# Performance work log

Measured on AMD Instinct MI355X. Metric: run time of the kernel, lower is better.

The kernel has to match this reference:

```python
import jax, jax.numpy as jnp
import numpy as np

B, TQ, TKV, D, H = 4, 512, 4096, 1024, 8
HEAD_DIM = D // H


def setup_inputs() -> dict:
    key = jax.random.key(0)
    ks = jax.random.split(key, 8)
    s = 0.02
    inputs_q = jax.random.normal(ks[0], (B, TQ, D), jnp.float32)
    inputs_kv = jax.random.normal(ks[1], (B, TKV, D), jnp.float32)
    attention_mask = jax.random.randint(ks[2], (B, TQ, TKV), 0, 2).astype(bool)
    Wq = jax.random.normal(ks[3], (D, D), jnp.float32) * s
    Wk = jax.random.normal(ks[4], (D, D), jnp.float32) * s
    Wv = jax.random.normal(ks[5], (D, D), jnp.float32) * s
    Wo = jax.random.normal(ks[6], (D, D), jnp.float32) * s
    zb = jnp.zeros((D,), jnp.float32)
    return {"inputs_q": inputs_q, "inputs_kv": inputs_kv, "attention_mask": attention_mask,
            "Wq": Wq, "bq": zb, "Wk": Wk, "bk": zb, "Wv": Wv, "bv": zb, "Wo": Wo, "bo": zb}


def _split_heads(x, h):
    b, t, c = x.shape
    return x.reshape(b, t, h, c // h).transpose(0, 2, 1, 3)  # b h t d


def reference(inputs_q, inputs_kv, attention_mask, Wq, bq, Wk, bk, Wv, bv, Wo, bo):
    q = _split_heads(inputs_q @ Wq + bq, H)   # [b,h,tq,d]
    k = _split_heads(inputs_kv @ Wk + bk, H)  # [b,h,tkv,d]
    v = _split_heads(inputs_kv @ Wv + bv, H)  # [b,h,tkv,d]
    scale = 1.0 / np.sqrt(HEAD_DIM).astype(np.float32)
    scores = jnp.einsum('bhtd,bhTd->bhtT', q, k) * scale
    large_k = jnp.asarray(1e30, scores.dtype)  # 1e30 for fp32 per source
    scores = jnp.where(attention_mask[:, None, :, :], scores, -large_k)
    probs = jax.nn.softmax(scores, axis=-1)
    summed = jnp.einsum('bhtT,bhTd->bhtd', probs, v)
    b, h, t, d = summed.shape
    summed = summed.transpose(0, 2, 1, 3).reshape(b, t, h * d)  # [b,tq,hiddens]
    # wipe rows whose mask is entirely zero (post-softmax wipe-masking)
    wipe = jnp.all(~attention_mask, axis=-1, keepdims=True)  # [b,tq,1]
    summed = jnp.where(wipe, jnp.zeros_like(summed), summed)
    return summed @ Wo + bo
```

## Files before the change

kernel.cpp:

```cpp
#include <hip/hip_runtime.h>
#include <cstdint>
#include <cstddef>

typedef unsigned short US;
typedef __bf16 bf16_t;
typedef bf16_t bf16x8 __attribute__((ext_vector_type(8)));
typedef float  f32x4  __attribute__((ext_vector_type(4)));
typedef US     us8    __attribute__((ext_vector_type(8)));
typedef US     us4    __attribute__((ext_vector_type(4)));

#define AS1 __attribute__((address_space(1)))
#define AS3 __attribute__((address_space(3)))

__device__ __forceinline__ void gl_lds16(const void* g, void* l) {
    __builtin_amdgcn_global_load_lds((AS1 unsigned int*)(size_t)g,
                                     (AS3 unsigned int*)l, 16, 0, 0);
}

__device__ __forceinline__ US f2bf(float f) {
    unsigned u = __builtin_bit_cast(unsigned, f);
    u += 0x7FFFu + ((u >> 16) & 1u);
    return (US)(u >> 16);
}

__device__ __forceinline__ bf16x8 ldv8(const US* p) {
    return __builtin_bit_cast(bf16x8, *(const us8*)p);
}

__global__ void conv_bf16(const float* __restrict__ in, US* __restrict__ out, int n4) {
    int i = blockIdx.x * blockDim.x + threadIdx.x;
    if (i < n4) {
        float4 f = ((const float4*)in)[i];
        us4 o = { f2bf(f.x), f2bf(f.y), f2bf(f.z), f2bf(f.w) };
        ((us4*)out)[i] = o;
    }
}

__global__ void conv_mask(const int* __restrict__ in, US* __restrict__ out, int n4) {
    int i = blockIdx.x * blockDim.x + threadIdx.x;
    if (i < n4) {
        int4 m = ((const int4*)in)[i];
        us4 o = { (US)(m.x ? 1 : 0), (US)(m.y ? 1 : 0),
                  (US)(m.z ? 1 : 0), (US)(m.w ? 1 : 0) };
        ((us4*)out)[i] = o;
    }
}

__global__ void wt_conv(const float* __restrict__ Wq, const float* __restrict__ Wk,
                        const float* __restrict__ Wv, const float* __restrict__ Wo,
                        US* __restrict__ outbase) {
    const float* W = (blockIdx.z == 0) ? Wq : (blockIdx.z == 1) ? Wk
                   : (blockIdx.z == 2) ? Wv : Wo;
    US* WT = outbase + (size_t)blockIdx.z * 1024 * 1024;
    __shared__ float t[32][33];
    int tx = threadIdx.x & 31, ty = threadIdx.x >> 5;
    int x = blockIdx.x * 32 + tx;
#pragma unroll
    for (int r = 0; r < 4; ++r)
        t[ty + r * 8][tx] = W[(size_t)(blockIdx.y * 32 + ty + r * 8) * 1024 + x];
    __syncthreads();
    int nx = blockIdx.y * 32 + tx;
#pragma unroll
    for (int r = 0; r < 4; ++r)
        WT[(size_t)(blockIdx.x * 32 + ty + r * 8) * 1024 + nx] = f2bf(t[tx][ty + r * 8]);
}

__global__ void v_transpose(const US* __restrict__ Vh, US* __restrict__ VTh) {
    __shared__ US t[32][33];
    int tx = threadIdx.x & 31, ty = threadIdx.x >> 5;
    size_t base = (size_t)blockIdx.z * 4096 * 128;
    int t0 = blockIdx.x * 32, d0 = blockIdx.y * 32;
#pragma unroll
    for (int r = 0; r < 4; ++r)
        t[ty + r * 8][tx] = Vh[base + (size_t)(t0 + ty + r * 8) * 128 + d0 + tx];
    __syncthreads();
#pragma unroll
    for (int r = 0; r < 4; ++r)
        VTh[base + (size_t)(d0 + ty + r * 8) * 4096 + t0 + tx] = t[tx][ty + r * 8];
}

template <int MODE>
__global__ __launch_bounds__(256, 2)
void gemm_bt(const US* __restrict__ A, const US* __restrict__ Bt,
             const float* __restrict__ bias, void* __restrict__ out,
             int tlog2, float scale) {
    constexpr int K = 1024, N = 1024, BK = 64;
    __shared__ US As[128 * BK];
    __shared__ US Bs[128 * BK];
    const int tid = threadIdx.x;
    const int wv = tid >> 6, ln = tid & 63;
    const int g = ln >> 4, c15 = ln & 15;
    const int m0 = blockIdx.x * 128, n0 = blockIdx.y * 128;
    const int wm = (wv & 1) * 64, wn = (wv >> 1) * 64;

    f32x4 acc[4][4];
    const f32x4 z = {0.f, 0.f, 0.f, 0.f};
#pragma unroll
    for (int i = 0; i < 4; ++i)
#pragma unroll
        for (int j = 0; j < 4; ++j) acc[i][j] = z;

    const US* Ab = A + (size_t)m0 * K;
    const US* Bb = Bt + (size_t)n0 * K;

    for (int k0 = 0; k0 < K; k0 += BK) {
        __syncthreads();
#pragma unroll
        for (int q = 0; q < 4; ++q) {
            int eb = (q * 256 + wv * 64) * 8;
            int r = (eb >> 6) + (ln >> 3);
            int sw = (ln & 7) ^ (r & 7);
            gl_lds16(Ab + (size_t)r * K + k0 + sw * 8, &As[eb]);
            gl_lds16(Bb + (size_t)r * K + k0 + sw * 8, &Bs[eb]);
        }
        __syncthreads();
#pragma unroll
        for (int ks = 0; ks < 2; ++ks) {
            bf16x8 a[4], b[4];
#pragma unroll
            for (int i = 0; i < 4; ++i) {
                int p = (ks * 4 + g) ^ (c15 & 7);
                a[i] = ldv8(&As[(wm + i * 16 + c15) * BK + p * 8]);
            }
#pragma unroll
            for (int j = 0; j < 4; ++j) {
                int p = (ks * 4 + g) ^ (c15 & 7);
                b[j] = ldv8(&Bs[(wn + j * 16 + c15) * BK + p * 8]);
            }
#pragma unroll
            for (int i = 0; i < 4; ++i)
#pragma unroll
                for (int j = 0; j < 4; ++j)
                    acc[i][j] = __builtin_amdgcn_mfma_f32_16x16x32_bf16(a[i], b[j], acc[i][j], 0, 0, 0);
        }
    }

#pragma unroll
    for (int i = 0; i < 4; ++i) {
#pragma unroll
        for (int j = 0; j < 4; ++j) {
            int col = n0 + wn + j * 16 + c15;
            float bvv = bias[col];
#pragma unroll
            for (int r = 0; r < 4; ++r) {
                int row = m0 + wm + i * 16 + g * 4 + r;
                float v = (acc[i][j][r] + bvv) * scale;
                if (MODE == 0) {
                    int b_ = row >> tlog2;
                    int t = row & ((1 << tlog2) - 1);
                    int h = col >> 7, d = col & 127;
                    ((US*)out)[(((size_t)(b_ * 8 + h) << tlog2) + t) * 128 + d] = f2bf(v);
                } else {
                    ((float*)out)[(size_t)row * N + col] = v;
                }
            }
        }
    }
}

__global__ __launch_bounds__(256, 2)
void gemm_kv(const US* __restrict__ A, const US* __restrict__ BtK,
             const US* __restrict__ BtV, const float* __restrict__ bk,
             const float* __restrict__ bv, US* __restrict__ Kout,
             US* __restrict__ Vout) {
    constexpr int K = 1024, BK = 64;
    __shared__ US As[128 * BK];
    __shared__ US BsK[128 * BK];
    __shared__ US BsV[128 * BK];
    const int tid = threadIdx.x;
    const int wv = tid >> 6, ln = tid & 63;
    const int g = ln >> 4, c15 = ln & 15;
    const int m0 = blockIdx.x * 128, n0 = blockIdx.y * 128;
    const int wm = (wv & 1) * 64, wn = (wv >> 1) * 64;

    f32x4 aK[4][4], aV[4][4];
    const f32x4 z = {0.f, 0.f, 0.f, 0.f};
#pragma unroll
    for (int i = 0; i < 4; ++i)
#pragma unroll
        for (int j = 0; j < 4; ++j) { aK[i][j] = z; aV[i][j] = z; }

    const US* Ab  = A   + (size_t)m0 * K;
    const US* BbK = BtK + (size_t)n0 * K;
    const US* BbV = BtV + (size_t)n0 * K;

    for (int k0 = 0; k0 < K; k0 += BK) {
        __syncthreads();
#pragma unroll
        for (int q = 0; q < 4; ++q) {
            int eb = (q * 256 + wv * 64) * 8;
            int r = (eb >> 6) + (ln >> 3);
            int sw = (ln & 7) ^ (r & 7);
            gl_lds16(Ab  + (size_t)r * K + k0 + sw * 8, &As[eb]);
            gl_lds16(BbK + (size_t)r * K + k0 + sw * 8, &BsK[eb]);
            gl_lds16(BbV + (size_t)r * K + k0 + sw * 8, &BsV[eb]);
        }
        __syncthreads();
#pragma unroll
        for (int ks = 0; ks < 2; ++ks) {
            bf16x8 a[4], bK[4], bV[4];
#pragma unroll
            for (int i = 0; i < 4; ++i) {
                int p = (ks * 4 + g) ^ (c15 & 7);
                a[i] = ldv8(&As[(wm + i * 16 + c15) * BK + p * 8]);
            }
#pragma unroll
            for (int j = 0; j < 4; ++j) {
                int p = (ks * 4 + g) ^ (c15 & 7);
                bK[j] = ldv8(&BsK[(wn + j * 16 + c15) * BK + p * 8]);
                bV[j] = ldv8(&BsV[(wn + j * 16 + c15) * BK + p * 8]);
            }
#pragma unroll
            for (int i = 0; i < 4; ++i)
#pragma unroll
                for (int j = 0; j < 4; ++j) {
                    aK[i][j] = __builtin_amdgcn_mfma_f32_16x16x32_bf16(a[i], bK[j], aK[i][j], 0, 0, 0);
                    aV[i][j] = __builtin_amdgcn_mfma_f32_16x16x32_bf16(a[i], bV[j], aV[i][j], 0, 0, 0);
                }
        }
    }

#pragma unroll
    for (int i = 0; i < 4; ++i) {
#pragma unroll
        for (int j = 0; j < 4; ++j) {
            int col = n0 + wn + j * 16 + c15;
            float bkv = bk[col], bvv = bv[col];
            int h = col >> 7, d = col & 127;
#pragma unroll
            for (int r = 0; r < 4; ++r) {
                int row = m0 + wm + i * 16 + g * 4 + r;
                int b_ = row >> 12, t = row & 4095;
                size_t oi = (((size_t)(b_ * 8 + h) << 12) + t) * 128 + d;
                Kout[oi] = f2bf(aK[i][j][r] + bkv);
                Vout[oi] = f2bf(aV[i][j][r] + bvv);
            }
        }
    }
}

__global__ __launch_bounds__(256, 3)
void flash(const US* __restrict__ Qh, const US* __restrict__ Kh,
           const US* __restrict__ VTh, const US* __restrict__ Mk,
           float* __restrict__ Opart, float* __restrict__ Lpart) {
    __shared__ US Ks[64 * 128];
    __shared__ US Vs[128 * 64];
    __shared__ US Qs[64 * 128];
    const int tid = threadIdx.x, wv = tid >> 6, ln = tid & 63;
    const int g = ln >> 4, c15 = ln & 15;
    const int qt = blockIdx.x, q0 = qt * 64;
    const int bh = blockIdx.y, b_ = bh >> 3;
    const int sp = blockIdx.z, kvbase = sp * 1024;
    const int wq = wv * 16;

    {
        const US* Qb = Qh + ((size_t)bh * 512 + q0) * 128;
#pragma unroll
        for (int q = 0; q < 4; ++q) {
            int eb = (q * 256 + wv * 64) * 8;
            int r = (eb >> 7) + (ln >> 4);
            int sw = (ln & 15) ^ (r & 15);
            gl_lds16(Qb + (size_t)r * 128 + sw * 8, &Qs[eb]);
        }
    }
    __syncthreads();
    bf16x8 qa[4];
#pragma unroll
    for (int s = 0; s < 4; ++s) {
        int p = (s * 4 + g) ^ c15;
        qa[s] = ldv8(&Qs[(wq + c15) * 128 + p * 8]);
    }
    __syncthreads();
    US* Pw = &Qs[wv * (16 * 64)];

    f32x4 o[8];
    const f32x4 z = {0.f, 0.f, 0.f, 0.f};
#pragma unroll
    for (int j = 0; j < 8; ++j) o[j] = z;
    float l4[4] = {0.f, 0.f, 0.f, 0.f};

    const US* mrow  = Mk + (size_t)(b_ * 512 + q0 + wq + g * 4) * 4096 + c15;
    const US* Kbase = Kh + (size_t)bh * 4096 * 128;
    const US* Vbase = VTh + (size_t)bh * 128 * 4096;

    for (int t = 0; t < 16; ++t) {
        int kv0 = kvbase + t * 64;
        __syncthreads();
        const US* Kb = Kbase + (size_t)kv0 * 128;
#pragma unroll
        for (int q = 0; q < 4; ++q) {
            int eb = (q * 256 + wv * 64) * 8;
            int r = (eb >> 7) + (ln >> 4);
            int sw = (ln & 15) ^ (r & 15);
            gl_lds16(Kb + (size_t)r * 128 + sw * 8, &Ks[eb]);
        }
#pragma unroll
        for (int q = 0; q < 4; ++q) {
            int eb = (q * 256 + wv * 64) * 8;
            int r = (eb >> 6) + (ln >> 3);
            int sw = (ln & 7) ^ (r & 7);
            gl_lds16(Vbase + (size_t)r * 4096 + kv0 + sw * 8, &Vs[eb]);
        }
        US mv[4][4];
#pragma unroll
        for (int r2 = 0; r2 < 4; ++r2) {
            const US* pr = mrow + (size_t)r2 * 4096 + kv0;
#pragma unroll
            for (int j = 0; j < 4; ++j) mv[r2][j] = pr[j * 16];
        }
        __syncthreads();

        f32x4 s[4];
#pragma unroll
        for (int j = 0; j < 4; ++j) s[j] = z;
#pragma unroll
        for (int ks = 0; ks < 4; ++ks) {
#pragma unroll
            for (int j = 0; j < 4; ++j) {
                int p = (ks * 4 + g) ^ c15;
                bf16x8 kb = ldv8(&Ks[(j * 16 + c15) * 128 + p * 8]);
                s[j] = __builtin_amdgcn_mfma_f32_16x16x32_bf16(qa[ks], kb, s[j], 0, 0, 0);
            }
        }
#pragma unroll
        for (int j = 0; j < 4; ++j) {
#pragma unroll
            for (int r2 = 0; r2 < 4; ++r2) {
                float pp = __expf(s[j][r2]);
                pp = mv[r2][j] ? pp : 0.0f;
                l4[r2] += pp;
                int m = g * 4 + r2;
                int c = (c15 >> 3) + j * 2;
                Pw[m * 64 + ((c ^ (m & 7)) * 8) + (c15 & 7)] = f2bf(pp);
            }
        }
#pragma unroll
        for (int ks = 0; ks < 2; ++ks) {
            int pp_ = (ks * 4 + g) ^ (c15 & 7);
            bf16x8 pa = ldv8(&Pw[c15 * 64 + pp_ * 8]);
#pragma unroll
            for (int j = 0; j < 8; ++j) {
                int pv = (ks * 4 + g) ^ (c15 & 7);
                bf16x8 vb = ldv8(&Vs[(j * 16 + c15) * 64 + pv * 8]);
                o[j] = __builtin_amdgcn_mfma_f32_16x16x32_bf16(pa, vb, o[j], 0, 0, 0);
            }
        }
    }

#pragma unroll
    for (int r = 0; r < 4; ++r) {
        float l = l4[r];
        l += __shfl_xor(l, 1); l += __shfl_xor(l, 2);
        l += __shfl_xor(l, 4); l += __shfl_xor(l, 8);
        l4[r] = l;
    }
    size_t obase = ((((size_t)sp * 32 + bh) * 8 + qt) * 64 + wq) * 128;
#pragma unroll
    for (int j = 0; j < 8; ++j)
#pragma unroll
        for (int r = 0; r < 4; ++r)
            Opart[obase + (size_t)(g * 4 + r) * 128 + j * 16 + c15] = o[j][r];
    if (c15 == 0) {
#pragma unroll
        for (int r = 0; r < 4; ++r)
            Lpart[(((size_t)sp * 32 + bh) * 8 + qt) * 64 + wq + g * 4 + r] = l4[r];
    }
}

__global__ void combine(const float* __restrict__ Opart, const float* __restrict__ Lpart,
                        US* __restrict__ AO) {
    const int bh = blockIdx.x >> 3, qt = blockIdx.x & 7;
    const int b_ = bh >> 3, h = bh & 7;
    const int tid = threadIdx.x;
    const size_t sstride = (size_t)32 * 8 * 64 * 128;
    const size_t lstride = (size_t)32 * 8 * 64;
    const size_t slice  = ((size_t)bh * 8 + qt) * 64 * 128;
    const size_t lslice = ((size_t)bh * 8 + qt) * 64;
#pragma unroll
    for (int i = 0; i < 8; ++i) {
        int p = tid + i * 256;
        int row = p >> 5;
        float lsum = Lpart[lslice + row] + Lpart[lstride + lslice + row]
                   + Lpart[2 * lstride + lslice + row] + Lpart[3 * lstride + lslice + row];
        float inv = lsum > 0.f ? 1.f / lsum : 0.f;
        float4 a = *((const float4*)(Opart + slice) + p);
        float4 b = *((const float4*)(Opart + sstride + slice) + p);
        float4 c = *((const float4*)(Opart + 2 * sstride + slice) + p);
        float4 d = *((const float4*)(Opart + 3 * sstride + slice) + p);
        float x = (a.x + b.x + c.x + d.x) * inv;
        float y = (a.y + b.y + c.y + d.y) * inv;
        float z2 = (a.z + b.z + c.z + d.z) * inv;
        float w = (a.w + b.w + c.w + d.w) * inv;
        int d_ = (p & 31) * 4;
        int trow = qt * 64 + row;
        us4 ov = { f2bf(x), f2bf(y), f2bf(z2), f2bf(w) };
        *(us4*)(AO + ((size_t)(b_ * 512 + trow)) * 1024 + h * 128 + d_) = ov;
    }
}

extern "C" void kernel_launch(void* const* d_in, const int* in_sizes, int n_in,
                              void* d_out, int out_size, void* d_ws, size_t ws_size,
                              hipStream_t stream) {
    (void)in_sizes; (void)n_in; (void)out_size; (void)ws_size;
    const float* Xq  = (const float*)d_in[0];
    const float* Xkv = (const float*)d_in[1];
    const int*   Mi  = (const int*)d_in[2];
    const float* Wq  = (const float*)d_in[3];
    const float* bq  = (const float*)d_in[4];
    const float* Wk  = (const float*)d_in[5];
    const float* bk  = (const float*)d_in[6];
    const float* Wv  = (const float*)d_in[7];
    const float* bv  = (const float*)d_in[8];
    const float* Wo  = (const float*)d_in[9];
    const float* bo  = (const float*)d_in[10];
    float* out = (float*)d_out;

    char* p = (char*)d_ws;
    US* XqB  = (US*)p; p += (size_t)2048 * 1024 * 2;
    US* XkvB = (US*)p; p += (size_t)16384 * 1024 * 2;
    US* WT   = (US*)p; p += (size_t)4 * 1024 * 1024 * 2;
    US* MB   = (US*)p; p += (size_t)4 * 512 * 4096 * 2;
    US* Qh   = (US*)p; p += (size_t)2048 * 1024 * 2;
    US* Kh   = (US*)p; p += (size_t)16384 * 1024 * 2;
    US* Vh   = (US*)p; p += (size_t)16384 * 1024 * 2;
    US* VTh  = (US*)p; p += (size_t)16384 * 1024 * 2;
    US* AO   = (US*)p; p += (size_t)2048 * 1024 * 2;
    float* Opart = (float*)XkvB;
    float* Lpart = (float*)Vh;

    conv_bf16<<<2048, 256, 0, stream>>>(Xq, XqB, 2048 * 1024 / 4);
    conv_bf16<<<16384, 256, 0, stream>>>(Xkv, XkvB, 16384 * 1024 / 4);
    conv_mask<<<8192, 256, 0, stream>>>(Mi, MB, 4 * 512 * 4096 / 4);
    wt_conv<<<dim3(32, 32, 4), 256, 0, stream>>>(Wq, Wk, Wv, Wo, WT);

    gemm_bt<0><<<dim3(16, 8), 256, 0, stream>>>(XqB, WT, bq, Qh, 9, 0.08838834764831843f);
    gemm_kv<<<dim3(128, 8), 256, 0, stream>>>(XkvB, WT + 1048576, WT + 2097152,
                                              bk, bv, Kh, Vh);
    v_transpose<<<dim3(128, 4, 32), 256, 0, stream>>>(Vh, VTh);
    flash<<<dim3(8, 32, 4), 256, 0, stream>>>(Qh, Kh, VTh, MB, Opart, Lpart);
    combine<<<256, 256, 0, stream>>>(Opart, Lpart, AO);
    gemm_bt<1><<<dim3(16, 8), 256, 0, stream>>>(AO, WT + 3145728, bo, out, 0, 1.0f);
}
```

Before: 382.3 us.

## Widen flash q-tile to 128, split KV six ways, fuse prep kernels

The flash kernel now gives each wave 32 query rows instead of 16, so every K/V tile loaded into LDS is reused across twice as many queries. Q fragments are loaded straight from global memory, and the KV range is split into 6 uneven chunks to keep the grid size reasonable. Partial outputs are stored transposed with vectorized mask loads, and combine uses an LDS transpose to reduce 6 partials. The three conversion kernels are merged into one launch. The cost is higher register pressure, since the kernel holds twice the accumulators, plus extra combine traffic from 6 partials instead of 4.

```diff
diff --git a/kernel.cpp b/kernel.cpp
--- a/kernel.cpp
+++ b/kernel.cpp
@@ -27,22 +27,26 @@
     return __builtin_bit_cast(bf16x8, *(const us8*)p);
 }
 
-__global__ void conv_bf16(const float* __restrict__ in, US* __restrict__ out, int n4) {
-    int i = blockIdx.x * blockDim.x + threadIdx.x;
-    if (i < n4) {
-        float4 f = ((const float4*)in)[i];
+__global__ void prep(const float* __restrict__ Xq, const float* __restrict__ Xkv,
+                     const int* __restrict__ Mi, US* __restrict__ XqB,
+                     US* __restrict__ XkvB, US* __restrict__ MB) {
+    int b = blockIdx.x, tid = threadIdx.x;
+    if (b < 2048) {
+        int i = b * 256 + tid;
+        float4 f = ((const float4*)Xq)[i];
         us4 o = { f2bf(f.x), f2bf(f.y), f2bf(f.z), f2bf(f.w) };
-        ((us4*)out)[i] = o;
-    }
-}
-
-__global__ void conv_mask(const int* __restrict__ in, US* __restrict__ out, int n4) {
-    int i = blockIdx.x * blockDim.x + threadIdx.x;
-    if (i < n4) {
-        int4 m = ((const int4*)in)[i];
+        ((us4*)XqB)[i] = o;
+    } else if (b < 18432) {
+        int i = (b - 2048) * 256 + tid;
+        float4 f = ((const float4*)Xkv)[i];
+        us4 o = { f2bf(f.x), f2bf(f.y), f2bf(f.z), f2bf(f.w) };
+        ((us4*)XkvB)[i] = o;
+    } else {
+        int i = (b - 18432) * 256 + tid;
+        int4 m = ((const int4*)Mi)[i];
         us4 o = { (US)(m.x ? 1 : 0), (US)(m.y ? 1 : 0),
                   (US)(m.z ? 1 : 0), (US)(m.w ? 1 : 0) };
-        ((us4*)out)[i] = o;
+        ((us4*)MB)[i] = o;
     }
 }
 
@@ -245,48 +249,42 @@
            float* __restrict__ Opart, float* __restrict__ Lpart) {
     __shared__ US Ks[64 * 128];
     __shared__ US Vs[128 * 64];
-    __shared__ US Qs[64 * 128];
+    __shared__ US Ps[4][32 * 64];
     const int tid = threadIdx.x, wv = tid >> 6, ln = tid & 63;
     const int g = ln >> 4, c15 = ln & 15;
-    const int qt = blockIdx.x, q0 = qt * 64;
+    const int qt = blockIdx.x, qbase = qt * 128;
     const int bh = blockIdx.y, b_ = bh >> 3;
-    const int sp = blockIdx.z, kvbase = sp * 1024;
-    const int wq = wv * 16;
-
-    {
-        const US* Qb = Qh + ((size_t)bh * 512 + q0) * 128;
-#pragma unroll
-        for (int q = 0; q < 4; ++q) {
-            int eb = (q * 256 + wv * 64) * 8;
-            int r = (eb >> 7) + (ln >> 4);
-            int sw = (ln & 15) ^ (r & 15);
-            gl_lds16(Qb + (size_t)r * 128 + sw * 8, &Qs[eb]);
-        }
-    }
-    __syncthreads();
-    bf16x8 qa[4];
-#pragma unroll
-    for (int s = 0; s < 4; ++s) {
-        int p = (s * 4 + g) ^ c15;
-        qa[s] = ldv8(&Qs[(wq + c15) * 128 + p * 8]);
-    }
-    __syncthreads();
-    US* Pw = &Qs[wv * (16 * 64)];
-
-    f32x4 o[8];
+    const int sp = blockIdx.z;
+    const int t0 = (sp < 4) ? sp * 11 : 44 + (sp - 4) * 10;
+    const int nt = (sp < 4) ? 11 : 10;
+    const int wq = wv * 32;
+
+    bf16x8 qa[2][4];
+#pragma unroll
+    for (int ib = 0; ib < 2; ++ib) {
+        const US* qrow = Qh + ((size_t)bh * 512 + qbase + wq + ib * 16 + c15) * 128;
+#pragma unroll
+        for (int ks = 0; ks < 4; ++ks)
+            qa[ib][ks] = ldv8(qrow + ks * 32 + g * 8);
+    }
+
+    f32x4 o[8][2];
     const f32x4 z = {0.f, 0.f, 0.f, 0.f};
 #pragma unroll
-    for (int j = 0; j < 8; ++j) o[j] = z;
-    float l4[4] = {0.f, 0.f, 0.f, 0.f};
-
-    const US* mrow  = Mk + (size_t)(b_ * 512 + q0 + wq + g * 4) * 4096 + c15;
-    const US* Kbase = Kh + (size_t)bh * 4096 * 128;
+    for (int d = 0; d < 8; ++d) { o[d][0] = z; o[d][1] = z; }
+    float l2[2] = {0.f, 0.f};
+
+    const US* mp[2];
+    mp[0] = Mk + (size_t)(b_ * 512 + qbase + wq + c15) * 4096;
+    mp[1] = mp[0] + (size_t)16 * 4096;
+    const US* Kbase = Kh + ((size_t)bh * 4096 + (size_t)t0 * 64) * 128;
     const US* Vbase = VTh + (size_t)bh * 128 * 4096;
-
-    for (int t = 0; t < 16; ++t) {
-        int kv0 = kvbase + t * 64;
-        __syncthreads();
-        const US* Kb = Kbase + (size_t)kv0 * 128;
+    US* Pw = &Ps[wv][0];
+
+    for (int t = 0; t < nt; ++t) {
+        int kv0 = (t0 + t) * 64;
+        __syncthreads();
+        const US* Kb = Kbase + (size_t)t * 64 * 128;
 #pragma unroll
         for (int q = 0; q < 4; ++q) {
             int eb = (q * 256 + wv * 64) * 8;
@@ -301,100 +299,123 @@
             int sw = (ln & 7) ^ (r & 7);
             gl_lds16(Vbase + (size_t)r * 4096 + kv0 + sw * 8, &Vs[eb]);
         }
-        US mv[4][4];
-#pragma unroll
-        for (int r2 = 0; r2 < 4; ++r2) {
-            const US* pr = mrow + (size_t)r2 * 4096 + kv0;
-#pragma unroll
-            for (int j = 0; j < 4; ++j) mv[r2][j] = pr[j * 16];
-        }
-        __syncthreads();
-
-        f32x4 s[4];
-#pragma unroll
-        for (int j = 0; j < 4; ++j) s[j] = z;
-#pragma unroll
-        for (int ks = 0; ks < 4; ++ks) {
-#pragma unroll
-            for (int j = 0; j < 4; ++j) {
-                int p = (ks * 4 + g) ^ c15;
-                bf16x8 kb = ldv8(&Ks[(j * 16 + c15) * 128 + p * 8]);
-                s[j] = __builtin_amdgcn_mfma_f32_16x16x32_bf16(qa[ks], kb, s[j], 0, 0, 0);
-            }
-        }
-#pragma unroll
-        for (int j = 0; j < 4; ++j) {
-#pragma unroll
-            for (int r2 = 0; r2 < 4; ++r2) {
-                float pp = __expf(s[j][r2]);
-                pp = mv[r2][j] ? pp : 0.0f;
-                l4[r2] += pp;
-                int m = g * 4 + r2;
-                int c = (c15 >> 3) + j * 2;
-                Pw[m * 64 + ((c ^ (m & 7)) * 8) + (c15 & 7)] = f2bf(pp);
-            }
-        }
+        us4 mv[2][4];
+#pragma unroll
+        for (int ib = 0; ib < 2; ++ib)
+#pragma unroll
+            for (int kb = 0; kb < 4; ++kb)
+                mv[ib][kb] = *(const us4*)(mp[ib] + kv0 + kb * 16 + g * 4);
+        __syncthreads();
+
+#pragma unroll
+        for (int kb = 0; kb < 4; ++kb) {
+            f32x4 s0 = z, s1 = z;
+#pragma unroll
+            for (int ks = 0; ks < 4; ++ks) {
+                bf16x8 kf = ldv8(&Ks[(kb * 16 + c15) * 128 + (((ks * 4 + g) ^ c15) * 8)]);
+                s0 = __builtin_amdgcn_mfma_f32_16x16x32_bf16(kf, qa[0][ks], s0, 0, 0, 0);
+                s1 = __builtin_amdgcn_mfma_f32_16x16x32_bf16(kf, qa[1][ks], s1, 0, 0, 0);
+            }
+            int cw = kb * 4 + g;
+#pragma unroll
+            for (int ib = 0; ib < 2; ++ib) {
+                f32x4 sv = ib ? s1 : s0;
+                float p0 = mv[ib][kb].x ? __expf(sv[0]) : 0.f;
+                float p1 = mv[ib][kb].y ? __expf(sv[1]) : 0.f;
+                float p2 = mv[ib][kb].z ? __expf(sv[2]) : 0.f;
+                float p3 = mv[ib][kb].w ? __expf(sv[3]) : 0.f;
+                l2[ib] += (p0 + p1) + (p2 + p3);
+                int q = ib * 16 + c15;
+                US* wp = Pw + q * 64 + (((cw >> 1) ^ (q & 7)) * 8) + (cw & 1) * 4;
+                us4 pv = { f2bf(p0), f2bf(p1), f2bf(p2), f2bf(p3) };
+                *(us4*)wp = pv;
+            }
+        }
+
 #pragma unroll
         for (int ks = 0; ks < 2; ++ks) {
-            int pp_ = (ks * 4 + g) ^ (c15 & 7);
-            bf16x8 pa = ldv8(&Pw[c15 * 64 + pp_ * 8]);
-#pragma unroll
-            for (int j = 0; j < 8; ++j) {
-                int pv = (ks * 4 + g) ^ (c15 & 7);
-                bf16x8 vb = ldv8(&Vs[(j * 16 + c15) * 64 + pv * 8]);
-                o[j] = __builtin_amdgcn_mfma_f32_16x16x32_bf16(pa, vb, o[j], 0, 0, 0);
-            }
-        }
-    }
-
-#pragma unroll
-    for (int r = 0; r < 4; ++r) {
-        float l = l4[r];
-        l += __shfl_xor(l, 1); l += __shfl_xor(l, 2);
-        l += __shfl_xor(l, 4); l += __shfl_xor(l, 8);
-        l4[r] = l;
-    }
-    size_t obase = ((((size_t)sp * 32 + bh) * 8 + qt) * 64 + wq) * 128;
-#pragma unroll
-    for (int j = 0; j < 8; ++j)
-#pragma unroll
-        for (int r = 0; r < 4; ++r)
-            Opart[obase + (size_t)(g * 4 + r) * 128 + j * 16 + c15] = o[j][r];
-    if (c15 == 0) {
-#pragma unroll
-        for (int r = 0; r < 4; ++r)
-            Lpart[(((size_t)sp * 32 + bh) * 8 + qt) * 64 + wq + g * 4 + r] = l4[r];
-    }
+            bf16x8 pf[2];
+#pragma unroll
+            for (int ib = 0; ib < 2; ++ib) {
+                int q = ib * 16 + c15;
+                pf[ib] = ldv8(&Pw[q * 64 + (((ks * 4 + g) ^ (q & 7)) * 8)]);
+            }
+#pragma unroll
+            for (int d = 0; d < 8; ++d) {
+                bf16x8 vf = ldv8(&Vs[(d * 16 + c15) * 64 + (((ks * 4 + g) ^ (c15 & 7)) * 8)]);
+                o[d][0] = __builtin_amdgcn_mfma_f32_16x16x32_bf16(vf, pf[0], o[d][0], 0, 0, 0);
+                o[d][1] = __builtin_amdgcn_mfma_f32_16x16x32_bf16(vf, pf[1], o[d][1], 0, 0, 0);
+            }
+        }
+    }
+
+    float lf[2];
+#pragma unroll
+    for (int ib = 0; ib < 2; ++ib) {
+        float l = l2[ib];
+        l += __shfl_xor(l, 16); l += __shfl_xor(l, 32);
+        lf[ib] = l;
+    }
+    if (ln < 16) {
+        size_t lb = ((size_t)sp * 32 + bh) * 512 + qbase + wq + c15;
+        Lpart[lb] = lf[0];
+        Lpart[lb + 16] = lf[1];
+    }
+    float* Ob = Opart + (((size_t)sp * 32 + bh) * 128 + g * 4) * 512 + qbase + wq + c15;
+#pragma unroll
+    for (int d = 0; d < 8; ++d)
+#pragma unroll
+        for (int r = 0; r < 4; ++r) {
+            Ob[(size_t)(d * 16 + r) * 512] = o[d][0][r];
+            Ob[(size_t)(d * 16 + r) * 512 + 16] = o[d][1][r];
+        }
 }
 
 __global__ void combine(const float* __restrict__ Opart, const float* __restrict__ Lpart,
                         US* __restrict__ AO) {
-    const int bh = blockIdx.x >> 3, qt = blockIdx.x & 7;
+    __shared__ float linv[128];
+    __shared__ float T[128 * 33];
+    const int qt = blockIdx.x, bh = blockIdx.y;
     const int b_ = bh >> 3, h = bh & 7;
     const int tid = threadIdx.x;
-    const size_t sstride = (size_t)32 * 8 * 64 * 128;
-    const size_t lstride = (size_t)32 * 8 * 64;
-    const size_t slice  = ((size_t)bh * 8 + qt) * 64 * 128;
-    const size_t lslice = ((size_t)bh * 8 + qt) * 64;
-#pragma unroll
-    for (int i = 0; i < 8; ++i) {
-        int p = tid + i * 256;
-        int row = p >> 5;
-        float lsum = Lpart[lslice + row] + Lpart[lstride + lslice + row]
-                   + Lpart[2 * lstride + lslice + row] + Lpart[3 * lstride + lslice + row];
-        float inv = lsum > 0.f ? 1.f / lsum : 0.f;
-        float4 a = *((const float4*)(Opart + slice) + p);
-        float4 b = *((const float4*)(Opart + sstride + slice) + p);
-        float4 c = *((const float4*)(Opart + 2 * sstride + slice) + p);
-        float4 d = *((const float4*)(Opart + 3 * sstride + slice) + p);
-        float x = (a.x + b.x + c.x + d.x) * inv;
-        float y = (a.y + b.y + c.y + d.y) * inv;
-        float z2 = (a.z + b.z + c.z + d.z) * inv;
-        float w = (a.w + b.w + c.w + d.w) * inv;
-        int d_ = (p & 31) * 4;
-        int trow = qt * 64 + row;
-        us4 ov = { f2bf(x), f2bf(y), f2bf(z2), f2bf(w) };
-        *(us4*)(AO + ((size_t)(b_ * 512 + trow)) * 1024 + h * 128 + d_) = ov;
+    const size_t spstride = (size_t)32 * 128 * 512;
+
+    if (tid < 128) {
+        float s = 0.f;
+#pragma unroll
+        for (int sp = 0; sp < 6; ++sp)
+            s += Lpart[((size_t)sp * 32 + bh) * 512 + qt * 128 + tid];
+        linv[tid] = (s > 0.f) ? 1.f / s : 0.f;
+    }
+    __syncthreads();
+
+    for (int ds0 = 0; ds0 < 128; ds0 += 32) {
+        if (ds0) __syncthreads();
+#pragma unroll
+        for (int it = 0; it < 4; ++it) {
+            int d = ds0 + (tid >> 5) + it * 8, qc = tid & 31;
+            const float* base = Opart + ((size_t)bh * 128 + d) * 512 + qt * 128 + qc * 4;
+            float4 a = {0.f, 0.f, 0.f, 0.f};
+#pragma unroll
+            for (int sp = 0; sp < 6; ++sp) {
+                float4 v = *(const float4*)(base + sp * spstride);
+                a.x += v.x; a.y += v.y; a.z += v.z; a.w += v.w;
+            }
+            int dd = d - ds0;
+            T[(qc * 4 + 0) * 33 + dd] = a.x * linv[qc * 4 + 0];
+            T[(qc * 4 + 1) * 33 + dd] = a.y * linv[qc * 4 + 1];
+            T[(qc * 4 + 2) * 33 + dd] = a.z * linv[qc * 4 + 2];
+            T[(qc * 4 + 3) * 33 + dd] = a.w * linv[qc * 4 + 3];
+        }
+        __syncthreads();
+#pragma unroll
+        for (int it = 0; it < 4; ++it) {
+            int idx = tid + it * 256;
+            int q = idx >> 3, c = idx & 7;
+            const float* tr = &T[q * 33 + c * 4];
+            us4 ov = { f2bf(tr[0]), f2bf(tr[1]), f2bf(tr[2]), f2bf(tr[3]) };
+            *(us4*)(AO + ((size_t)(b_ * 512 + qt * 128 + q)) * 1024 + h * 128 + ds0 + c * 4) = ov;
+        }
     }
 }
 
@@ -416,28 +437,26 @@
     float* out = (float*)d_out;
 
     char* p = (char*)d_ws;
+    US* WT   = (US*)p; p += (size_t)4 * 1024 * 1024 * 2;
+    US* AO   = (US*)p; p += (size_t)2048 * 1024 * 2;
     US* XqB  = (US*)p; p += (size_t)2048 * 1024 * 2;
-    US* XkvB = (US*)p; p += (size_t)16384 * 1024 * 2;
-    US* WT   = (US*)p; p += (size_t)4 * 1024 * 1024 * 2;
-    US* MB   = (US*)p; p += (size_t)4 * 512 * 4096 * 2;
     US* Qh   = (US*)p; p += (size_t)2048 * 1024 * 2;
     US* Kh   = (US*)p; p += (size_t)16384 * 1024 * 2;
+    US* VTh  = (US*)p; p += (size_t)16384 * 1024 * 2;
+    US* XkvB = (US*)p; p += (size_t)16384 * 1024 * 2;
     US* Vh   = (US*)p; p += (size_t)16384 * 1024 * 2;
-    US* VTh  = (US*)p; p += (size_t)16384 * 1024 * 2;
-    US* AO   = (US*)p; p += (size_t)2048 * 1024 * 2;
+    US* MB   = (US*)p; p += (size_t)4 * 512 * 4096 * 2;
     float* Opart = (float*)XkvB;
-    float* Lpart = (float*)Vh;
-
-    conv_bf16<<<2048, 256, 0, stream>>>(Xq, XqB, 2048 * 1024 / 4);
-    conv_bf16<<<16384, 256, 0, stream>>>(Xkv, XkvB, 16384 * 1024 / 4);
-    conv_mask<<<8192, 256, 0, stream>>>(Mi, MB, 4 * 512 * 4096 / 4);
+    float* Lpart = (float*)XqB;
+
+    prep<<<26624, 256, 0, stream>>>(Xq, Xkv, Mi, XqB, XkvB, MB);
     wt_conv<<<dim3(32, 32, 4), 256, 0, stream>>>(Wq, Wk, Wv, Wo, WT);
 
     gemm_bt<0><<<dim3(16, 8), 256, 0, stream>>>(XqB, WT, bq, Qh, 9, 0.08838834764831843f);
     gemm_kv<<<dim3(128, 8), 256, 0, stream>>>(XkvB, WT + 1048576, WT + 2097152,
                                               bk, bv, Kh, Vh);
     v_transpose<<<dim3(128, 4, 32), 256, 0, stream>>>(Vh, VTh);
-    flash<<<dim3(8, 32, 4), 256, 0, stream>>>(Qh, Kh, VTh, MB, Opart, Lpart);
-    combine<<<256, 256, 0, stream>>>(Opart, Lpart, AO);
+    flash<<<dim3(4, 32, 6), 256, 0, stream>>>(Qh, Kh, VTh, MB, Opart, Lpart);
+    combine<<<dim3(4, 32), 256, 0, stream>>>(Opart, Lpart, AO);
     gemm_bt<1><<<dim3(16, 8), 256, 0, stream>>>(AO, WT + 3145728, bo, out, 0, 1.0f);
 }
```

Result: faster. 353.6 us (-7.5%).
